# Performance work log

Measured on AMD Instinct MI355X. Metric: run time of the kernel, lower is better.

Reference implementation:

```python
import jax, jax.numpy as jnp
import numpy as np
import math

IN_FEATURES = 4096
OUT_FEATURES = 4096
NUM_COMPONENTS = 256
TWO_PI = 2.0 * math.pi


def setup_inputs() -> dict:
    key = jax.random.key(0)
    k1, k2, k3, k4 = jax.random.split(key, 4)
    x = jax.random.normal(k1, (4096, IN_FEATURES), dtype=jnp.float32)
    mus = jax.random.uniform(k2, (NUM_COMPONENTS, 2), dtype=jnp.float32)
    log_vars = -3.0 - jax.random.uniform(k3, (NUM_COMPONENTS, 2), dtype=jnp.float32)
    weights = jax.random.uniform(k4, (NUM_COMPONENTS,), dtype=jnp.float32) / NUM_COMPONENTS
    return {"x": x, "mus": mus, "log_vars": log_vars, "weights": weights}


def reference(x, mus, log_vars, weights):
    in_features = x.shape[1]
    x_in_idx = jnp.linspace(0.0, 1.0, in_features, dtype=jnp.float32)    # [I]
    x_out_idx = jnp.linspace(0.0, 1.0, OUT_FEATURES, dtype=jnp.float32)  # [O]
    vars_ = jnp.exp(log_vars)  # [M, 2]

    # Input-side Gaussian basis, fused with 1/sqrt(2*pi*var) and component weight: [I, M]
    d_in = (x_in_idx[:, None] - mus[None, :, 0]) ** 2
    G_in = jnp.exp(-d_in / (2.0 * vars_[None, :, 0])) / jnp.sqrt(TWO_PI * vars_[None, :, 0]) * weights[None, :]
    C = x @ G_in  # [B, M]

    # Output-side Gaussian pdf (Normal(mu1, sigma1).log_prob(x_out).exp()): [M, O]
    d_out = (x_out_idx[None, :] - mus[:, 1:2]) ** 2
    G_out = jnp.exp(-d_out / (2.0 * vars_[:, 1:2])) / jnp.sqrt(TWO_PI * vars_[:, 1:2])

    x_out = (C @ G_out) / (in_features * jnp.sum(weights))  # [B, O]
    return x_out
```

## Files before the change

kernel.cpp:

```cpp
#include <hip/hip_runtime.h>
#include <hip/hip_bf16.h>
#include <math.h>

#define IN_FEAT 4096
#define OUT_FEAT 4096
#define NCOMP 256
#define BATCH 4096
#define TWO_PI_F 6.28318530717958647692f

typedef __attribute__((ext_vector_type(8))) short short8;
typedef __attribute__((ext_vector_type(8))) __bf16 bf16x8;
typedef __attribute__((ext_vector_type(4))) float f32x4;
typedef __attribute__((ext_vector_type(16))) float f32x16;

__device__ __forceinline__ ushort f2b(float f) {
  union { float f; unsigned u; } v; v.f = f;
  unsigned r = (v.u + 0x7fffu + ((v.u >> 16) & 1u)) >> 16;
  return (ushort)r;
}

__device__ __forceinline__ float b2f(short s) {
  union { unsigned u; float f; } v; v.u = ((unsigned)(ushort)s) << 16;
  return v.f;
}

__device__ __forceinline__ bf16x8 ld_frag(const void* p) {
  short8 s = *(const short8*)p;
  return __builtin_bit_cast(bf16x8, s);
}

__device__ __forceinline__ bf16x8 cvt8f(float4 a, float4 b) {
  bf16x8 r;
  r[0] = (__bf16)a.x; r[1] = (__bf16)a.y; r[2] = (__bf16)a.z; r[3] = (__bf16)a.w;
  r[4] = (__bf16)b.x; r[5] = (__bf16)b.y; r[6] = (__bf16)b.z; r[7] = (__bf16)b.w;
  return r;
}

__device__ __forceinline__ void gload_lds16(const void* g, void* l) {
  __builtin_amdgcn_global_load_lds(
      (const __attribute__((address_space(1))) void*)g,
      (__attribute__((address_space(3))) void*)l, 16, 0, 0);
}

__global__ __launch_bounds__(256) void prep_kernel(
    const float* __restrict__ mus, const float* __restrict__ lvs,
    const float* __restrict__ w,
    ushort* __restrict__ Gt, ushort* __restrict__ GoT) {
  int idx = blockIdx.x * 256 + threadIdx.x;
  if (idx < NCOMP * IN_FEAT) {
    int m = idx >> 12, i = idx & (IN_FEAT - 1);
    float v = expf(lvs[2 * m]);
    float d = (float)i * (1.0f / (IN_FEAT - 1)) - mus[2 * m];
    float g = expf(-d * d * (0.5f / v)) * rsqrtf(TWO_PI_F * v) * w[m];
    Gt[idx] = f2b(g);
  } else {
    idx -= NCOMP * IN_FEAT;
    int o = idx >> 8, m = idx & (NCOMP - 1);
    float v = expf(lvs[2 * m + 1]);
    float d = (float)o * (1.0f / (OUT_FEAT - 1)) - mus[2 * m + 1];
    float g = expf(-d * d * (0.5f / v)) * rsqrtf(TWO_PI_F * v);
    GoT[idx] = f2b(g);
  }
}

template<int NS>
__global__ __launch_bounds__(256, 1) void gemm1_kernel(
    const float* __restrict__ x, const ushort* __restrict__ Gt,
    ushort* __restrict__ Cpart) {
  constexpr int KR = IN_FEAT / NS;
  constexpr int NT = KR / 32;
  __shared__ __align__(16) ushort Bs[NT * 8192];
  const int tid = threadIdx.x, wid = tid >> 6, lane = tid & 63;
  const int l15 = lane & 15, q = lane >> 4;
  const int m0 = blockIdx.x * 256;
  const int kb0 = blockIdx.y * KR;

  {
    const int brow = lane >> 2;
    const int bsw = (((lane & 3) ^ ((lane >> 3) & 3)) << 3);
    #pragma unroll
    for (int i = 0; i < 32; ++i) {
      int idx = wid * 32 + i;
      int seg = idx >> 4, nf = idx & 15;
      gload_lds16(&Gt[(size_t)(nf * 16 + brow) * IN_FEAT + kb0 + seg * 32 + bsw],
                  &Bs[seg * 8192 + nf * 512]);
    }
  }
  __syncthreads();

  const int fswz = (q << 4) ^ (((l15 >> 1) & 3) << 4);
  ushort* Cp = Cpart + (size_t)blockIdx.y * ((size_t)BATCH * NCOMP);

  for (int g = 0; g < 2; ++g) {
    const int rb0 = m0 + ((g * 2 + 0) * 4 + wid) * 16;
    const int rb1 = m0 + ((g * 2 + 1) * 4 + wid) * 16;
    const float* xa = &x[(size_t)(rb0 + l15) * IN_FEAT + kb0 + q * 8];
    const float* xb = &x[(size_t)(rb1 + l15) * IN_FEAT + kb0 + q * 8];

    f32x4 acc0[16] = {}, acc1[16] = {};
    float4 ea0, ea1, eb0, eb1, oa0, oa1, ob0, ob1;
    ea0 = *(const float4*)(xa);     ea1 = *(const float4*)(xa + 4);
    eb0 = *(const float4*)(xb);     eb1 = *(const float4*)(xb + 4);

    #define COMP(T, A0, A1, B0, B1) {                                        \
      bf16x8 af0 = cvt8f(A0, A1);                                            \
      bf16x8 af1 = cvt8f(B0, B1);                                            \
      const char* sb = (const char*)Bs + (T) * 16384;                        \
      _Pragma("unroll")                                                      \
      for (int nf = 0; nf < 16; ++nf) {                                      \
        bf16x8 bf = ld_frag(sb + (nf * 16 + l15) * 64 + fswz);               \
        acc0[nf] = __builtin_amdgcn_mfma_f32_16x16x32_bf16(af0, bf, acc0[nf], 0, 0, 0); \
        acc1[nf] = __builtin_amdgcn_mfma_f32_16x16x32_bf16(af1, bf, acc1[nf], 0, 0, 0); \
      } }

    #pragma unroll
    for (int t = 0; t < NT; t += 2) {
      oa0 = *(const float4*)(xa + (t + 1) * 32);
      oa1 = *(const float4*)(xa + (t + 1) * 32 + 4);
      ob0 = *(const float4*)(xb + (t + 1) * 32);
      ob1 = *(const float4*)(xb + (t + 1) * 32 + 4);
      COMP(t, ea0, ea1, eb0, eb1)
      const int t2 = (t + 2 < NT) ? (t + 2) : (NT - 2);
      ea0 = *(const float4*)(xa + t2 * 32);
      ea1 = *(const float4*)(xa + t2 * 32 + 4);
      eb0 = *(const float4*)(xb + t2 * 32);
      eb1 = *(const float4*)(xb + t2 * 32 + 4);
      COMP(t + 1, oa0, oa1, ob0, ob1)
    }
    #undef COMP

    #pragma unroll
    for (int nf = 0; nf < 16; ++nf)
      #pragma unroll
      for (int r = 0; r < 4; ++r) {
        int col = nf * 16 + l15;
        Cp[(size_t)(rb0 + q * 4 + r) * NCOMP + col] = f2b(acc0[nf][r]);
        Cp[(size_t)(rb1 + q * 4 + r) * NCOMP + col] = f2b(acc1[nf][r]);
      }
  }
}

template<int NS>
__global__ __launch_bounds__(256) void reduce_kernel(ushort* __restrict__ Cp) {
  size_t i = ((size_t)blockIdx.x * 256 + threadIdx.x) * 8;
  float s[8] = {};
  #pragma unroll
  for (int p = 0; p < NS; ++p) {
    short8 v = *(const short8*)&Cp[(size_t)p * BATCH * NCOMP + i];
    #pragma unroll
    for (int e = 0; e < 8; ++e) s[e] += b2f(v[e]);
  }
  short8 hh;
  #pragma unroll
  for (int e = 0; e < 8; ++e) hh[e] = (short)f2b(s[e]);
  *(short8*)&Cp[i] = hh;
}

__global__ __launch_bounds__(256, 4) void gemm2_kernel(
    const ushort* __restrict__ Cb, const ushort* __restrict__ GoT,
    const float* __restrict__ w, float* __restrict__ out) {
  __shared__ __align__(16) ushort lds[2 * 8192];
  const int tid = threadIdx.x, wid = tid >> 6, lane = tid & 63;
  const int m0 = blockIdx.y * 128, n0 = blockIdx.x * 128;
  const int wr = (wid >> 1) * 64, wc = (wid & 1) * 64;
  const int r32 = lane & 31, h = lane >> 5;

  float4 wv = *(const float4*)&w[lane * 4];
  float s = wv.x + wv.y + wv.z + wv.w;
  #pragma unroll
  for (int off = 32; off > 0; off >>= 1) s += __shfl_xor(s, off);
  const float scale = 1.0f / ((float)IN_FEAT * s);

  const int brow = lane >> 2;
  const int bswz = (((lane & 3) ^ ((lane >> 3) & 3)) << 3);
  const int sw0 = (h << 4) ^ (((r32 >> 1) & 3) << 4);

  f32x16 acc[2][2] = {};

  #define STAGE2(buf, k0)                                                    \
    _Pragma("unroll")                                                        \
    for (int q2 = 0; q2 < 2; ++q2) {                                         \
      int c = wid * 2 + q2;                                                  \
      int row = c * 16 + brow;                                               \
      gload_lds16(&Cb[(size_t)(m0 + row) * NCOMP + (k0) + bswz],             \
                  &lds[(buf) * 8192 + c * 512]);                             \
      gload_lds16(&GoT[(size_t)(n0 + row) * NCOMP + (k0) + bswz],            \
                  &lds[(buf) * 8192 + 4096 + c * 512]);                      \
    }

  STAGE2(0, 0)
  __syncthreads();

  for (int t = 0; t < 8; ++t) {
    if (t < 7) STAGE2((t + 1) & 1, (t + 1) * 32)
    const char* base = (const char*)lds + (t & 1) * 16384;
    const char* Bb = base + 8192;
    #pragma unroll
    for (int s2 = 0; s2 < 2; ++s2) {
      const int off = sw0 ^ (s2 << 5);
      bf16x8 a0 = ld_frag(base + (wr + r32) * 64 + off);
      bf16x8 a1 = ld_frag(base + (wr + 32 + r32) * 64 + off);
      bf16x8 b0 = ld_frag(Bb + (wc + r32) * 64 + off);
      bf16x8 b1 = ld_frag(Bb + (wc + 32 + r32) * 64 + off);
      acc[0][0] = __builtin_amdgcn_mfma_f32_32x32x16_bf16(a0, b0, acc[0][0], 0, 0, 0);
      acc[0][1] = __builtin_amdgcn_mfma_f32_32x32x16_bf16(a0, b1, acc[0][1], 0, 0, 0);
      acc[1][0] = __builtin_amdgcn_mfma_f32_32x32x16_bf16(a1, b0, acc[1][0], 0, 0, 0);
      acc[1][1] = __builtin_amdgcn_mfma_f32_32x32x16_bf16(a1, b1, acc[1][1], 0, 0, 0);
    }
    __syncthreads();
  }
  #undef STAGE2

  #pragma unroll
  for (int mi = 0; mi < 2; ++mi)
    #pragma unroll
    for (int nj = 0; nj < 2; ++nj)
      #pragma unroll
      for (int g = 0; g < 16; ++g) {
        int row = m0 + wr + mi * 32 + (g & 3) + 8 * (g >> 2) + 4 * h;
        int col = n0 + wc + nj * 32 + r32;
        out[(size_t)row * OUT_FEAT + col] = acc[mi][nj][g] * scale;
      }
}

extern "C" void kernel_launch(void* const* d_in, const int* in_sizes, int n_in,
                              void* d_out, int out_size, void* d_ws, size_t ws_size,
                              hipStream_t stream) {
  const float* x   = (const float*)d_in[0];
  const float* mus = (const float*)d_in[1];
  const float* lvs = (const float*)d_in[2];
  const float* w   = (const float*)d_in[3];
  float* out = (float*)d_out;

  ushort* Gt  = (ushort*)d_ws;
  ushort* GoT = Gt  + (size_t)NCOMP * IN_FEAT;
  ushort* Cpart = GoT + (size_t)OUT_FEAT * NCOMP;

  prep_kernel<<<(NCOMP * IN_FEAT + OUT_FEAT * NCOMP) / 256, 256, 0, stream>>>(
      mus, lvs, w, Gt, GoT);

  gemm1_kernel<16><<<dim3(BATCH / 256, 16), 256, 0, stream>>>(x, Gt, Cpart);
  reduce_kernel<16><<<BATCH * NCOMP / 8 / 256, 256, 0, stream>>>(Cpart);

  gemm2_kernel<<<dim3(OUT_FEAT / 128, BATCH / 128), 256, 0, stream>>>(
      Cpart, GoT, w, out);
}
```

Before: 66.26 us.

## Double threads per gemm1 block and deepen x prefetch to four stages

gemm1 now runs 512 threads (8 waves) per block, and each wave handles 32 rows in a single pass instead of two sequential passes of 4 waves. The shared B tile load is split across the 8 waves. The x fragments are prefetched four k-steps ahead in a register ring, and the first loads are issued before the barrier. The aim is more latency hiding from extra waves and deeper prefetch of the global x loads. The cost is higher register pressure under launch_bounds(512,2), with 128 accumulator floats plus 64 prefetch floats per thread, which risks spills or lower occupancy.

```diff
diff --git a/kernel.cpp b/kernel.cpp
--- a/kernel.cpp
+++ b/kernel.cpp
@@ -64,7 +64,7 @@
 }
 
 template<int NS>
-__global__ __launch_bounds__(256, 1) void gemm1_kernel(
+__global__ __launch_bounds__(512, 2) void gemm1_kernel(
     const float* __restrict__ x, const ushort* __restrict__ Gt,
     ushort* __restrict__ Cpart) {
   constexpr int KR = IN_FEAT / NS;
@@ -79,65 +79,61 @@
     const int brow = lane >> 2;
     const int bsw = (((lane & 3) ^ ((lane >> 3) & 3)) << 3);
     #pragma unroll
-    for (int i = 0; i < 32; ++i) {
-      int idx = wid * 32 + i;
+    for (int i = 0; i < 16; ++i) {
+      int idx = wid * 16 + i;
       int seg = idx >> 4, nf = idx & 15;
       gload_lds16(&Gt[(size_t)(nf * 16 + brow) * IN_FEAT + kb0 + seg * 32 + bsw],
                   &Bs[seg * 8192 + nf * 512]);
     }
   }
+
+  const int rb0 = m0 + wid * 32;
+  const int rb1 = rb0 + 16;
+  const float* xa = &x[(size_t)(rb0 + l15) * IN_FEAT + kb0 + q * 8];
+  const float* xb = &x[(size_t)(rb1 + l15) * IN_FEAT + kb0 + q * 8];
+
+  float4 P[4][4];
+  #pragma unroll
+  for (int s = 0; s < 4; ++s) {
+    P[s][0] = *(const float4*)(xa + s * 32);
+    P[s][1] = *(const float4*)(xa + s * 32 + 4);
+    P[s][2] = *(const float4*)(xb + s * 32);
+    P[s][3] = *(const float4*)(xb + s * 32 + 4);
+  }
+
   __syncthreads();
 
+  f32x4 acc0[16] = {}, acc1[16] = {};
   const int fswz = (q << 4) ^ (((l15 >> 1) & 3) << 4);
+
+  #pragma unroll
+  for (int t = 0; t < NT; ++t) {
+    bf16x8 af0 = cvt8f(P[t & 3][0], P[t & 3][1]);
+    bf16x8 af1 = cvt8f(P[t & 3][2], P[t & 3][3]);
+    if (t + 4 < NT) {
+      P[t & 3][0] = *(const float4*)(xa + (t + 4) * 32);
+      P[t & 3][1] = *(const float4*)(xa + (t + 4) * 32 + 4);
+      P[t & 3][2] = *(const float4*)(xb + (t + 4) * 32);
+      P[t & 3][3] = *(const float4*)(xb + (t + 4) * 32 + 4);
+    }
+    const char* sb = (const char*)Bs + t * 16384;
+    #pragma unroll
+    for (int nf = 0; nf < 16; ++nf) {
+      bf16x8 bf = ld_frag(sb + (nf * 16 + l15) * 64 + fswz);
+      acc0[nf] = __builtin_amdgcn_mfma_f32_16x16x32_bf16(af0, bf, acc0[nf], 0, 0, 0);
+      acc1[nf] = __builtin_amdgcn_mfma_f32_16x16x32_bf16(af1, bf, acc1[nf], 0, 0, 0);
+    }
+  }
+
   ushort* Cp = Cpart + (size_t)blockIdx.y * ((size_t)BATCH * NCOMP);
-
-  for (int g = 0; g < 2; ++g) {
-    const int rb0 = m0 + ((g * 2 + 0) * 4 + wid) * 16;
-    const int rb1 = m0 + ((g * 2 + 1) * 4 + wid) * 16;
-    const float* xa = &x[(size_t)(rb0 + l15) * IN_FEAT + kb0 + q * 8];
-    const float* xb = &x[(size_t)(rb1 + l15) * IN_FEAT + kb0 + q * 8];
-
-    f32x4 acc0[16] = {}, acc1[16] = {};
-    float4 ea0, ea1, eb0, eb1, oa0, oa1, ob0, ob1;
-    ea0 = *(const float4*)(xa);     ea1 = *(const float4*)(xa + 4);
-    eb0 = *(const float4*)(xb);     eb1 = *(const float4*)(xb + 4);
-
-    #define COMP(T, A0, A1, B0, B1) {                                        \
-      bf16x8 af0 = cvt8f(A0, A1);                                            \
-      bf16x8 af1 = cvt8f(B0, B1);                                            \
-      const char* sb = (const char*)Bs + (T) * 16384;                        \
-      _Pragma("unroll")                                                      \
-      for (int nf = 0; nf < 16; ++nf) {                                      \
-        bf16x8 bf = ld_frag(sb + (nf * 16 + l15) * 64 + fswz);               \
-        acc0[nf] = __builtin_amdgcn_mfma_f32_16x16x32_bf16(af0, bf, acc0[nf], 0, 0, 0); \
-        acc1[nf] = __builtin_amdgcn_mfma_f32_16x16x32_bf16(af1, bf, acc1[nf], 0, 0, 0); \
-      } }
-
-    #pragma unroll
-    for (int t = 0; t < NT; t += 2) {
-      oa0 = *(const float4*)(xa + (t + 1) * 32);
-      oa1 = *(const float4*)(xa + (t + 1) * 32 + 4);
-      ob0 = *(const float4*)(xb + (t + 1) * 32);
-      ob1 = *(const float4*)(xb + (t + 1) * 32 + 4);
-      COMP(t, ea0, ea1, eb0, eb1)
-      const int t2 = (t + 2 < NT) ? (t + 2) : (NT - 2);
-      ea0 = *(const float4*)(xa + t2 * 32);
-      ea1 = *(const float4*)(xa + t2 * 32 + 4);
-      eb0 = *(const float4*)(xb + t2 * 32);
-      eb1 = *(const float4*)(xb + t2 * 32 + 4);
-      COMP(t + 1, oa0, oa1, ob0, ob1)
-    }
-    #undef COMP
-
-    #pragma unroll
-    for (int nf = 0; nf < 16; ++nf)
-      #pragma unroll
-      for (int r = 0; r < 4; ++r) {
-        int col = nf * 16 + l15;
-        Cp[(size_t)(rb0 + q * 4 + r) * NCOMP + col] = f2b(acc0[nf][r]);
-        Cp[(size_t)(rb1 + q * 4 + r) * NCOMP + col] = f2b(acc1[nf][r]);
-      }
-  }
+  #pragma unroll
+  for (int nf = 0; nf < 16; ++nf)
+    #pragma unroll
+    for (int r = 0; r < 4; ++r) {
+      int col = nf * 16 + l15;
+      Cp[(size_t)(rb0 + q * 4 + r) * NCOMP + col] = f2b(acc0[nf][r]);
+      Cp[(size_t)(rb1 + q * 4 + r) * NCOMP + col] = f2b(acc1[nf][r]);
+    }
 }
 
 template<int NS>
@@ -239,7 +235,7 @@
   prep_kernel<<<(NCOMP * IN_FEAT + OUT_FEAT * NCOMP) / 256, 256, 0, stream>>>(
       mus, lvs, w, Gt, GoT);
 
-  gemm1_kernel<16><<<dim3(BATCH / 256, 16), 256, 0, stream>>>(x, Gt, Cpart);
+  gemm1_kernel<16><<<dim3(BATCH / 256, 16), 512, 0, stream>>>(x, Gt, Cpart);
   reduce_kernel<16><<<BATCH * NCOMP / 8 / 256, 256, 0, stream>>>(Cpart);
 
   gemm2_kernel<<<dim3(OUT_FEAT / 128, BATCH / 128), 256, 0, stream>>>(
```

New measurement: 65.19 us. Within noise of the previous version (-1.6%).
